# Optimization experiments

Hardware: AMD Instinct MI355X
Metric: run time of the kernel (lower is better)

Reference implementation:

```python
import jax, jax.numpy as jnp
import numpy as np

N = 100000      # nodes
E = 3200000     # edges (avg degree 32)
IN_CH = 32
EDGE_DIM = 11
HID = IN_CH + 4 + EDGE_DIM   # 47
OUT = 128


def setup_inputs() -> dict:
    key = jax.random.key(0)
    ks = jax.random.split(key, 10)
    x = jax.random.normal(ks[0], (N, IN_CH), dtype=jnp.float32)
    pos = jax.random.normal(ks[1], (N, 3), dtype=jnp.float32) * 10.0
    nrm = jax.random.normal(ks[2], (N, 3), dtype=jnp.float32)
    normal = nrm / jnp.linalg.norm(nrm, axis=1, keepdims=True)
    # edges with src != dst (avoids degenerate zero-distance point pairs)
    src = jax.random.randint(ks[3], (E,), 0, N)
    off = jax.random.randint(ks[4], (E,), 1, N)
    dst = (src + off) % N
    edge_index = jnp.stack([src, dst], axis=0).astype(jnp.int64)
    edge_attr = jax.random.normal(ks[5], (E, EDGE_DIM), dtype=jnp.float32)
    W1 = jax.random.normal(ks[6], (HID, HID), dtype=jnp.float32) / np.sqrt(HID)
    b1 = jnp.zeros((HID,), dtype=jnp.float32)
    g1 = jnp.ones((HID,), dtype=jnp.float32)
    be1 = jnp.zeros((HID,), dtype=jnp.float32)
    W2 = jax.random.normal(ks[7], (HID, OUT), dtype=jnp.float32) / np.sqrt(HID)
    b2 = jnp.zeros((OUT,), dtype=jnp.float32)
    g2 = jnp.ones((OUT,), dtype=jnp.float32)
    be2 = jnp.zeros((OUT,), dtype=jnp.float32)
    return {"x": x, "pos": pos, "normal": normal, "edge_attr": edge_attr,
            "W1": W1, "b1": b1, "g1": g1, "be1": be1,
            "W2": W2, "b2": b2, "g2": g2, "be2": be2,
            "edge_index": edge_index}


def _angle(v1, v2):
    return jnp.arctan2(jnp.linalg.norm(jnp.cross(v1, v2), axis=1),
                       jnp.sum(v1 * v2, axis=1))


def _layernorm(h, g, b, eps=1e-5):
    mu = jnp.mean(h, axis=-1, keepdims=True)
    var = jnp.var(h, axis=-1, keepdims=True)  # biased, matches torch LayerNorm
    return (h - mu) / jnp.sqrt(var + eps) * g + b


def reference(x, pos, normal, edge_attr, W1, b1, g1, be1, W2, b2, g2, be2, edge_index):
    src, dst = edge_index[0], edge_index[1]  # message flows src(j) -> dst(i)
    pos_i, pos_j = pos[dst], pos[src]
    n_i, n_j = normal[dst], normal[src]
    x_j = x[src]
    pseudo = pos_j - pos_i                                  # [E,3]
    ppf = jnp.stack([jnp.linalg.norm(pseudo, axis=1),
                     _angle(n_i, pseudo),
                     _angle(n_j, pseudo),
                     _angle(n_i, n_j)], axis=1)             # [E,4]
    msg = jnp.concatenate([x_j, ppf, edge_attr], axis=1)    # [E,47]
    # local_nn = MLP([47,47,128]): (Lin->ReLU->LayerNorm->Dropout(eval)) x2
    h = _layernorm(jax.nn.relu(msg @ W1 + b1), g1, be1)     # [E,47]
    h = _layernorm(jax.nn.relu(h @ W2 + b2), g2, be2)       # [E,128]
    out = jax.ops.segment_max(h, dst, num_segments=N)       # scatter-max per target node
    return jnp.where(jnp.isfinite(out), out, 0.0)           # nodes w/o edges -> 0
```

## Files before the change

kernel.cpp:

```cpp
#include <hip/hip_runtime.h>
#include <cstdint>
#include <cstddef>


typedef _Float16 f16x8 __attribute__((ext_vector_type(8)));
typedef _Float16 f16x2 __attribute__((ext_vector_type(2)));
typedef float    f32x4 __attribute__((ext_vector_type(4)));

#define ENC_NEGINF 0x007FFFFFu
#define LDK 64
#define LDH 132

__device__ __forceinline__ int swz(int row, int col) {
    return (col & 7) | ((((col >> 3) ^ row) & 7) << 3);
}

__device__ __forceinline__ unsigned fenc(float f) {
    unsigned u = __float_as_uint(f);
    return (u & 0x80000000u) ? ~u : (u | 0x80000000u);
}

__global__ void init_out_kernel(unsigned* __restrict__ out, int n4) {
    int i = blockIdx.x * blockDim.x + threadIdx.x;
    if (i < n4)
        ((uint4*)out)[i] = make_uint4(ENC_NEGINF, ENC_NEGINF, ENC_NEGINF, ENC_NEGINF);
}

__global__ void finalize_out_kernel(float* __restrict__ out, int n) {
    int i = blockIdx.x * blockDim.x + threadIdx.x;
    if (i < n) {
        unsigned k = __float_as_uint(out[i]);
        float r;
        if (k == ENC_NEGINF) r = 0.0f;
        else {
            unsigned u = (k & 0x80000000u) ? (k ^ 0x80000000u) : ~k;
            r = __uint_as_float(u);
        }
        out[i] = r;
    }
}

__global__ void zero_kernel(int* __restrict__ p, int n) {
    int i = blockIdx.x * blockDim.x + threadIdx.x;
    if (i < n) p[i] = 0;
}

__global__ void hist_kernel(const int* __restrict__ dstI, int* __restrict__ counts, int E) {
    int i = blockIdx.x * blockDim.x + threadIdx.x;
    if (i < E) atomicAdd(&counts[dstI[i]], 1);
}

__global__ __launch_bounds__(1024) void scan_blk(const int* __restrict__ in,
                                                 int* __restrict__ outp,
                                                 int* __restrict__ bsums, int N) {
    __shared__ int wsum[16];
    const int tid = threadIdx.x, lane = tid & 63, wid = tid >> 6;
    int i = blockIdx.x * 1024 + tid;
    int v = (i < N) ? in[i] : 0;
    int incl = v;
#pragma unroll
    for (int m = 1; m < 64; m <<= 1) {
        int t = __shfl_up(incl, m, 64);
        if (lane >= m) incl += t;
    }
    if (lane == 63) wsum[wid] = incl;
    __syncthreads();
    int woff = 0;
#pragma unroll
    for (int k = 0; k < 16; ++k) woff += (k < wid) ? wsum[k] : 0;
    if (i < N) outp[i] = woff + incl - v;
    if (tid == 1023 && bsums != nullptr) bsums[blockIdx.x] = woff + incl;
}

__global__ __launch_bounds__(1024) void scan_add(int* __restrict__ outp,
                                                 const int* __restrict__ bsums, int N) {
    int i = blockIdx.x * 1024 + threadIdx.x;
    if (i < N) outp[i] += bsums[blockIdx.x];
}

__global__ void scatter_kernel(const int* __restrict__ srcI, const int* __restrict__ dstI,
                               int* __restrict__ nextp,
                               int2* __restrict__ se, int* __restrict__ dst_g, int E) {
    int i = blockIdx.x * blockDim.x + threadIdx.x;
    if (i < E) {
        int d = dstI[i];
        int p = atomicAdd(&nextp[d], 1);
        se[p] = make_int2(srcI[i], i);
        dst_g[p] = d;
    }
}

__global__ __launch_bounds__(512, 4) void edge_kernel_csr(
    const float* __restrict__ x,   const float* __restrict__ pos,
    const float* __restrict__ nrm, const float* __restrict__ ea,
    const float* __restrict__ W1,  const float* __restrict__ b1,
    const float* __restrict__ g1,  const float* __restrict__ be1,
    const float* __restrict__ W2,  const float* __restrict__ b2,
    const float* __restrict__ g2,  const float* __restrict__ be2,
    const int2* __restrict__ se,   const int* __restrict__ dst_g,
    unsigned* __restrict__ out, int E, int ntiles, int tilesPerBlock)
{
    __shared__ _Float16 W1t[48][LDK];
    __shared__ _Float16 W2t[128][LDK];
    __shared__ _Float16 msgA[128][LDK];
    __shared__ _Float16 h2w[128][LDH];
    __shared__ int dstL[128];

    const int lane = threadIdx.x & 63;
    const int w    = threadIdx.x >> 6;
    const int c16  = lane & 15;
    const int g    = lane >> 4;
    const int row0 = w * 16;

    for (int i = threadIdx.x; i < 48 * 64; i += 512) {
        int n = i >> 6, k = i & 63;
        W1t[n][swz(n, k)] = (n < 47 && k < 47) ? (_Float16)W1[k * 47 + n] : (_Float16)0.f;
    }
    for (int i = threadIdx.x; i < 128 * 64; i += 512) {
        int n = i >> 6, k = i & 63;
        W2t[n][swz(n, k)] = (k < 47) ? (_Float16)W2[k * 128 + n] : (_Float16)0.f;
    }
    for (int i = threadIdx.x; i < 128 * LDK; i += 512)
        (&msgA[0][0])[i] = (_Float16)0.f;

    float b1v[3], g1v[3], be1v[3];
#pragma unroll
    for (int n = 0; n < 3; ++n) {
        int cc = n * 16 + c16;
        bool vld = cc < 47;
        b1v[n]  = vld ? b1[cc]  : 0.f;
        g1v[n]  = vld ? g1[cc]  : 0.f;
        be1v[n] = vld ? be1[cc] : 0.f;
    }
    float b2v[8], g2v[8], be2v[8];
#pragma unroll
    for (int n = 0; n < 8; ++n) {
        int cc = n * 16 + c16;
        b2v[n] = b2[cc]; g2v[n] = g2[cc]; be2v[n] = be2[cc];
    }
    __syncthreads();

    const int xr = lane >> 2;
    const int xc = (lane & 3) * 8;
    const int eg = lane / 11, ec = lane - eg * 11;
    const bool ea_act  = lane < 44;
    const bool geo_act = lane < 48;

    const int tbeg = blockIdx.x * tilesPerBlock;
    int tend = tbeg + tilesPerBlock;
    if (tend > ntiles) tend = ntiles;

    for (int tile = tbeg; tile < tend; ++tile) {
        const int base = tile * 128 + row0;

        {
            int p = base + xr;
            bool vx = p < E;
            int s = vx ? se[p].x : 0;
            const float4* xp = (const float4*)(x + (size_t)s * 32 + xc);
            float4 xa = xp[0];
            float4 xb = xp[1];

            float eav0 = 0.f, eav1 = 0.f, eav2 = 0.f, eav3 = 0.f;
            if (ea_act) {
                int p0 = base + 0 * 4 + eg, p1 = base + 1 * 4 + eg;
                int p2 = base + 2 * 4 + eg, p3 = base + 3 * 4 + eg;
                int e0 = (p0 < E) ? se[p0].y : 0;
                int e1 = (p1 < E) ? se[p1].y : 0;
                int e2 = (p2 < E) ? se[p2].y : 0;
                int e3 = (p3 < E) ? se[p3].y : 0;
                eav0 = (p0 < E) ? ea[(size_t)e0 * 11 + ec] : 0.f;
                eav1 = (p1 < E) ? ea[(size_t)e1 * 11 + ec] : 0.f;
                eav2 = (p2 < E) ? ea[(size_t)e2 * 11 + ec] : 0.f;
                eav3 = (p3 < E) ? ea[(size_t)e3 * 11 + ec] : 0.f;
            }

            float gpix = 0.f, gpiy = 0.f, gpiz = 0.f;
            float gpjx = 0.f, gpjy = 0.f, gpjz = 0.f;
            float gnix = 0.f, gniy = 0.f, gniz = 0.f;
            float gnjx = 0.f, gnjy = 0.f, gnjz = 0.f;
            int pd = -1;
            if (geo_act) {
                int pg = base + c16;
                bool v = pg < E;
                int s2 = v ? se[pg].x : 0;
                int d2 = v ? dst_g[pg] : 0;
                pd = v ? d2 : -1;
                gpix = pos[d2 * 3 + 0]; gpiy = pos[d2 * 3 + 1]; gpiz = pos[d2 * 3 + 2];
                gpjx = pos[s2 * 3 + 0]; gpjy = pos[s2 * 3 + 1]; gpjz = pos[s2 * 3 + 2];
                gnix = nrm[d2 * 3 + 0]; gniy = nrm[d2 * 3 + 1]; gniz = nrm[d2 * 3 + 2];
                gnjx = nrm[s2 * 3 + 0]; gnjy = nrm[s2 * 3 + 1]; gnjz = nrm[s2 * 3 + 2];
            }

            {
                int r = row0 + xr;
                f16x8 hv;
                hv[0] = (_Float16)(vx ? xa.x : 0.f); hv[1] = (_Float16)(vx ? xa.y : 0.f);
                hv[2] = (_Float16)(vx ? xa.z : 0.f); hv[3] = (_Float16)(vx ? xa.w : 0.f);
                hv[4] = (_Float16)(vx ? xb.x : 0.f); hv[5] = (_Float16)(vx ? xb.y : 0.f);
                hv[6] = (_Float16)(vx ? xb.z : 0.f); hv[7] = (_Float16)(vx ? xb.w : 0.f);
                *(f16x8*)&msgA[r][swz(r, xc)] = hv;
            }
            if (ea_act) {
                int r0 = row0 + 0 * 4 + eg; msgA[r0][swz(r0, 36 + ec)] = (_Float16)eav0;
                int r1 = row0 + 1 * 4 + eg; msgA[r1][swz(r1, 36 + ec)] = (_Float16)eav1;
                int r2 = row0 + 2 * 4 + eg; msgA[r2][swz(r2, 36 + ec)] = (_Float16)eav2;
                int r3 = row0 + 3 * 4 + eg; msgA[r3][swz(r3, 36 + ec)] = (_Float16)eav3;
            }
            if (geo_act) {
                int r = row0 + c16;
                float px = gpjx - gpix, py = gpjy - gpiy, pz = gpjz - gpiz;
                float v1x, v1y, v1z, v2x, v2y, v2z;
                if (g == 0)      { v1x = gnix; v1y = gniy; v1z = gniz; v2x = px;   v2y = py;   v2z = pz; }
                else if (g == 1) { v1x = gnjx; v1y = gnjy; v1z = gnjz; v2x = px;   v2y = py;   v2z = pz; }
                else             { v1x = gnix; v1y = gniy; v1z = gniz; v2x = gnjx; v2y = gnjy; v2z = gnjz; }
                float cx = v1y * v2z - v1z * v2y;
                float cy = v1z * v2x - v1x * v2z;
                float cz = v1x * v2y - v1y * v2x;
                float ang = atan2f(sqrtf(cx * cx + cy * cy + cz * cz),
                                   v1x * v2x + v1y * v2y + v1z * v2z);
                msgA[r][swz(r, 33 + g)] = (_Float16)ang;
                if (g == 0) {
                    msgA[r][swz(r, 32)] = (_Float16)sqrtf(px * px + py * py + pz * pz);
                    dstL[r] = pd;
                }
            }
        }

        f32x4 acc1[3];
#pragma unroll
        for (int n = 0; n < 3; ++n) acc1[n] = (f32x4){0.f, 0.f, 0.f, 0.f};
#pragma unroll
        for (int ks = 0; ks < 2; ++ks) {
            int ar = row0 + c16;
            f16x8 a = *(const f16x8*)&msgA[ar][swz(ar, ks * 32 + g * 8)];
#pragma unroll
            for (int n = 0; n < 3; ++n) {
                int br = n * 16 + c16;
                f16x8 b = *(const f16x8*)&W1t[br][swz(br, ks * 32 + g * 8)];
                acc1[n] = __builtin_amdgcn_mfma_f32_16x16x32_f16(a, b, acc1[n], 0, 0, 0);
            }
        }
#pragma unroll
        for (int q = 0; q < 4; ++q) {
            float t0 = fmaxf(acc1[0][q] + b1v[0], 0.f);
            float t1 = fmaxf(acc1[1][q] + b1v[1], 0.f);
            float t2 = fmaxf(acc1[2][q] + b1v[2], 0.f);
            float s = t0 + t1 + t2;
            float s2 = t0 * t0 + t1 * t1 + t2 * t2;
#pragma unroll
            for (int m = 1; m < 16; m <<= 1) {
                s  += __shfl_xor(s,  m, 64);
                s2 += __shfl_xor(s2, m, 64);
            }
            float mu  = s * (1.f / 47.f);
            float var = s2 * (1.f / 47.f) - mu * mu;
            float rs  = rsqrtf(var + 1e-5f);
            int r = row0 + 4 * g + q;
            msgA[r][swz(r, c16)]      = (_Float16)((t0 - mu) * rs * g1v[0] + be1v[0]);
            msgA[r][swz(r, 16 + c16)] = (_Float16)((t1 - mu) * rs * g1v[1] + be1v[1]);
            msgA[r][swz(r, 32 + c16)] = (_Float16)((t2 - mu) * rs * g1v[2] + be1v[2]);
        }

        f32x4 acc2[8];
#pragma unroll
        for (int n = 0; n < 8; ++n) acc2[n] = (f32x4){0.f, 0.f, 0.f, 0.f};
#pragma unroll
        for (int ks = 0; ks < 2; ++ks) {
            int ar = row0 + c16;
            f16x8 a = *(const f16x8*)&msgA[ar][swz(ar, ks * 32 + g * 8)];
#pragma unroll
            for (int n = 0; n < 8; ++n) {
                int br = n * 16 + c16;
                f16x8 b = *(const f16x8*)&W2t[br][swz(br, ks * 32 + g * 8)];
                acc2[n] = __builtin_amdgcn_mfma_f32_16x16x32_f16(a, b, acc2[n], 0, 0, 0);
            }
        }
#pragma unroll
        for (int q = 0; q < 4; ++q) {
            float t[8];
            float s = 0.f, s2 = 0.f;
#pragma unroll
            for (int n = 0; n < 8; ++n) {
                t[n] = fmaxf(acc2[n][q] + b2v[n], 0.f);
                s += t[n]; s2 += t[n] * t[n];
            }
#pragma unroll
            for (int m = 1; m < 16; m <<= 1) {
                s  += __shfl_xor(s,  m, 64);
                s2 += __shfl_xor(s2, m, 64);
            }
            float mu  = s * (1.f / 128.f);
            float var = s2 * (1.f / 128.f) - mu * mu;
            float rs  = rsqrtf(var + 1e-5f);
            int r = row0 + 4 * g + q;
#pragma unroll
            for (int n = 0; n < 8; ++n) {
                float o = (t[n] - mu) * rs * g2v[n] + be2v[n];
                h2w[r][n * 16 + c16] = (_Float16)o;
            }
        }

        {
            float m0 = -INFINITY, m1 = -INFINITY;
            int segStart = 0;
            int dcur = dstL[row0];
#pragma unroll
            for (int r = 0; r < 16; ++r) {
                f16x2 pk = *(const f16x2*)&h2w[row0 + r][lane * 2];
                m0 = fmaxf(m0, (float)pk[0]);
                m1 = fmaxf(m1, (float)pk[1]);
                int dnext = (r < 15) ? dstL[row0 + r + 1] : -2;
                if (dnext != dcur) {
                    if (dcur >= 0) {
                        unsigned e0 = fenc(m0), e1 = fenc(m1);
                        unsigned* orow = out + (size_t)dcur * 128 + lane * 2;
                        if (segStart > 0 && r < 15) {
                            unsigned long long pk2 =
                                ((unsigned long long)e1 << 32) | (unsigned long long)e0;
                            *(unsigned long long*)orow = pk2;
                        } else {
                            atomicMax(orow,     e0);
                            atomicMax(orow + 1, e1);
                        }
                    }
                    m0 = -INFINITY; m1 = -INFINITY;
                    segStart = r + 1; dcur = dnext;
                }
            }
        }
    }
}

#define LDKF 72
__global__ __launch_bounds__(256) void edge_kernel_atomic(
    const float* __restrict__ x,   const float* __restrict__ pos,
    const float* __restrict__ nrm, const float* __restrict__ ea,
    const float* __restrict__ W1,  const float* __restrict__ b1,
    const float* __restrict__ g1,  const float* __restrict__ be1,
    const float* __restrict__ W2,  const float* __restrict__ b2,
    const float* __restrict__ g2,  const float* __restrict__ be2,
    const int* __restrict__ srcI,  const int* __restrict__ dstI,
    unsigned* __restrict__ out, int E, int ntiles)
{
    __shared__ _Float16 W1t[48][LDKF];
    __shared__ _Float16 W2t[128][LDKF];
    __shared__ _Float16 msgA[64][LDKF];
    __shared__ int dst_s[64];

    const int lane = threadIdx.x & 63;
    const int w    = threadIdx.x >> 6;
    const int c16  = lane & 15;
    const int g    = lane >> 4;

    for (int i = threadIdx.x; i < 48 * 64; i += 256) {
        int n = i >> 6, k = i & 63;
        W1t[n][k] = (n < 47 && k < 47) ? (_Float16)W1[k * 47 + n] : (_Float16)0.f;
    }
    for (int i = threadIdx.x; i < 128 * 64; i += 256) {
        int n = i >> 6, k = i & 63;
        W2t[n][k] = (k < 47) ? (_Float16)W2[k * 128 + n] : (_Float16)0.f;
    }
    for (int i = threadIdx.x; i < 64 * LDKF; i += 256)
        (&msgA[0][0])[i] = (_Float16)0.f;

    float b1v[3], g1v[3], be1v[3];
#pragma unroll
    for (int n = 0; n < 3; ++n) {
        int cc = n * 16 + c16;
        bool vld = cc < 47;
        b1v[n]  = vld ? b1[cc]  : 0.f;
        g1v[n]  = vld ? g1[cc]  : 0.f;
        be1v[n] = vld ? be1[cc] : 0.f;
    }
    float b2v[8], g2v[8], be2v[8];
#pragma unroll
    for (int n = 0; n < 8; ++n) {
        int cc = n * 16 + c16;
        b2v[n] = b2[cc]; g2v[n] = g2[cc]; be2v[n] = be2[cc];
    }
    __syncthreads();

    for (int tile = blockIdx.x; tile < ntiles; tile += gridDim.x) {
        const int base = tile * 64 + w * 16;
        const int row0 = w * 16;
#pragma unroll
        for (int i = 0; i < 8; ++i) {
            int el = i * 2 + (lane >> 5);
            int e  = base + el;
            int c  = lane & 31;
            float v = 0.f;
            if (e < E) v = x[(size_t)srcI[e] * 32 + c];
            msgA[row0 + el][c] = (_Float16)v;
        }
        if (lane < 44) {
            int eg = lane / 11, c = lane - eg * 11;
#pragma unroll
            for (int i = 0; i < 4; ++i) {
                int el = i * 4 + eg;
                int e  = base + el;
                float v = 0.f;
                if (e < E) v = ea[(size_t)e * 11 + c];
                msgA[row0 + el][36 + c] = (_Float16)v;
            }
        }
        if (lane < 48) {
            int el = c16;
            int e  = base + el;
            int s = 0, d = 0;
            bool vld = e < E;
            if (vld) { s = srcI[e]; d = dstI[e]; }
            float pix = pos[d * 3 + 0], piy = pos[d * 3 + 1], piz = pos[d * 3 + 2];
            float pjx = pos[s * 3 + 0], pjy = pos[s * 3 + 1], pjz = pos[s * 3 + 2];
            float nix = nrm[d * 3 + 0], niy = nrm[d * 3 + 1], niz = nrm[d * 3 + 2];
            float njx = nrm[s * 3 + 0], njy = nrm[s * 3 + 1], njz = nrm[s * 3 + 2];
            float px = pjx - pix, py = pjy - piy, pz = pjz - piz;
            float v1x, v1y, v1z, v2x, v2y, v2z;
            if (g == 0)      { v1x = nix; v1y = niy; v1z = niz; v2x = px;  v2y = py;  v2z = pz;  }
            else if (g == 1) { v1x = njx; v1y = njy; v1z = njz; v2x = px;  v2y = py;  v2z = pz;  }
        else             { v1x = nix; v1y = niy; v1z = niz; v2x = njx; v2y = njy; v2z = njz; }
            float cx = v1y * v2z - v1z * v2y;
            float cy = v1z * v2x - v1x * v2z;
            float cz = v1x * v2y - v1y * v2x;
            float ang = atan2f(sqrtf(cx * cx + cy * cy + cz * cz),
                               v1x * v2x + v1y * v2y + v1z * v2z);
            msgA[row0 + el][33 + g] = (_Float16)ang;
            if (g == 0) {
                msgA[row0 + el][32] = (_Float16)sqrtf(px * px + py * py + pz * pz);
                dst_s[row0 + el] = vld ? d : -1;
            }
        }

        f32x4 acc1[3];
#pragma unroll
        for (int n = 0; n < 3; ++n) acc1[n] = (f32x4){0.f, 0.f, 0.f, 0.f};
#pragma unroll
        for (int ks = 0; ks < 2; ++ks) {
            f16x8 a = *(const f16x8*)&msgA[row0 + c16][ks * 32 + g * 8];
#pragma unroll
            for (int n = 0; n < 3; ++n) {
                f16x8 b = *(const f16x8*)&W1t[n * 16 + c16][ks * 32 + g * 8];
                acc1[n] = __builtin_amdgcn_mfma_f32_16x16x32_f16(a, b, acc1[n], 0, 0, 0);
            }
        }
#pragma unroll
        for (int q = 0; q < 4; ++q) {
            float t0 = fmaxf(acc1[0][q] + b1v[0], 0.f);
            float t1 = fmaxf(acc1[1][q] + b1v[1], 0.f);
            float t2 = fmaxf(acc1[2][q] + b1v[2], 0.f);
            float s = t0 + t1 + t2;
            float s2 = t0 * t0 + t1 * t1 + t2 * t2;
#pragma unroll
            for (int m = 1; m < 16; m <<= 1) {
                s  += __shfl_xor(s,  m, 64);
                s2 += __shfl_xor(s2, m, 64);
            }
            float mu  = s * (1.f / 47.f);
            float var = s2 * (1.f / 47.f) - mu * mu;
            float rs  = rsqrtf(var + 1e-5f);
            int r = row0 + 4 * g + q;
            msgA[r][c16]      = (_Float16)((t0 - mu) * rs * g1v[0] + be1v[0]);
            msgA[r][16 + c16] = (_Float16)((t1 - mu) * rs * g1v[1] + be1v[1]);
            msgA[r][32 + c16] = (_Float16)((t2 - mu) * rs * g1v[2] + be1v[2]);
        }

        f32x4 acc2[8];
#pragma unroll
        for (int n = 0; n < 8; ++n) acc2[n] = (f32x4){0.f, 0.f, 0.f, 0.f};
#pragma unroll
        for (int ks = 0; ks < 2; ++ks) {
            f16x8 a = *(const f16x8*)&msgA[row0 + c16][ks * 32 + g * 8];
#pragma unroll
            for (int n = 0; n < 8; ++n) {
                f16x8 b = *(const f16x8*)&W2t[n * 16 + c16][ks * 32 + g * 8];
                acc2[n] = __builtin_amdgcn_mfma_f32_16x16x32_f16(a, b, acc2[n], 0, 0, 0);
            }
        }
        int4 dd = *(const int4*)&dst_s[row0 + 4 * g];
#pragma unroll
        for (int q = 0; q < 4; ++q) {
            float t[8];
            float s = 0.f, s2 = 0.f;
#pragma unroll
            for (int n = 0; n < 8; ++n) {
                t[n] = fmaxf(acc2[n][q] + b2v[n], 0.f);
                s += t[n]; s2 += t[n] * t[n];
            }
#pragma unroll
            for (int m = 1; m < 16; m <<= 1) {
                s  += __shfl_xor(s,  m, 64);
                s2 += __shfl_xor(s2, m, 64);
            }
            float mu  = s * (1.f / 128.f);
            float var = s2 * (1.f / 128.f) - mu * mu;
            float rs  = rsqrtf(var + 1e-5f);
            int d = (&dd.x)[q];
            if (d >= 0) {
                unsigned* orow = out + (size_t)d * 128u;
#pragma unroll
                for (int n = 0; n < 8; ++n) {
                    float o = (t[n] - mu) * rs * g2v[n] + be2v[n];
                    atomicMax(orow + n * 16 + c16, fenc(o));
                }
            }
        }
    }
}

extern "C" void kernel_launch(void* const* d_in, const int* in_sizes, int n_in,
                              void* d_out, int out_size, void* d_ws, size_t ws_size,
                              hipStream_t stream) {
    const float* x   = (const float*)d_in[0];
    const float* pos = (const float*)d_in[1];
    const float* nrm = (const float*)d_in[2];
    const float* ea  = (const float*)d_in[3];
    const float* W1  = (const float*)d_in[4];
    const float* b1  = (const float*)d_in[5];
    const float* g1  = (const float*)d_in[6];
    const float* be1 = (const float*)d_in[7];
    const float* W2  = (const float*)d_in[8];
    const float* b2  = (const float*)d_in[9];
    const float* g2  = (const float*)d_in[10];
    const float* be2 = (const float*)d_in[11];
    const int*   idx = (const int*)d_in[12];

    const int N = in_sizes[0] / 32;
    const int E = in_sizes[3] / 11;
    const int* srcI = idx;
    const int* dstI = idx + E;

    unsigned* outU = (unsigned*)d_out;
    const int n = N * 128;

    init_out_kernel<<<(n / 4 + 255) / 256, 256, 0, stream>>>(outU, n / 4);

    const int nb = (N + 1023) / 1024;
    const size_t needed = (size_t)E * 8 + (size_t)(2LL * N + E + nb) * 4;

    if (ws_size >= needed) {
        int2* se     = (int2*)d_ws;
        int*  counts = (int*)(se + E);
        int*  nextp  = counts + N;
        int*  dst_g  = nextp + N;
        int*  bsums  = dst_g + E;

        zero_kernel<<<(N + 255) / 256, 256, 0, stream>>>(counts, N);
        hist_kernel<<<(E + 255) / 256, 256, 0, stream>>>(dstI, counts, E);
        scan_blk<<<nb, 1024, 0, stream>>>(counts, nextp, bsums, N);
        scan_blk<<<1, 1024, 0, stream>>>(bsums, bsums, (int*)nullptr, nb);
        scan_add<<<nb, 1024, 0, stream>>>(nextp, bsums, N);
        scatter_kernel<<<(E + 255) / 256, 256, 0, stream>>>(srcI, dstI, nextp,
                                                            se, dst_g, E);

        const int ntiles = (E + 127) / 128;
        int grid = ntiles < 512 ? ntiles : 512;
        int tpb  = (ntiles + grid - 1) / grid;
        edge_kernel_csr<<<grid, 512, 0, stream>>>(x, pos, nrm, ea,
                                                  W1, b1, g1, be1,
                                                  W2, b2, g2, be2,
                                                  se, dst_g,
                                                  outU, E, ntiles, tpb);
    } else {
        const int ntiles = (E + 63) / 64;
        int grid = ntiles < 4096 ? ntiles : 4096;
        edge_kernel_atomic<<<grid, 256, 0, stream>>>(x, pos, nrm, ea,
                                                     W1, b1, g1, be1,
                                                     W2, b2, g2, be2,
                                                     srcI, dstI, outU, E, ntiles);
    }

    finalize_out_kernel<<<(n + 255) / 256, 256, 0, stream>>>((float*)d_out, n);
}
```

Measured before the change: 919.5 us.

## Keep MLP weights in registers, fold biases into GEMM, shrink CSR tiles

```diff
diff --git a/kernel.cpp b/kernel.cpp
--- a/kernel.cpp
+++ b/kernel.cpp
@@ -4,6 +4,7 @@
 
 
 typedef _Float16 f16x8 __attribute__((ext_vector_type(8)));
+typedef _Float16 f16x4 __attribute__((ext_vector_type(4)));
 typedef _Float16 f16x2 __attribute__((ext_vector_type(2)));
 typedef float    f32x4 __attribute__((ext_vector_type(4)));
 
@@ -90,7 +91,7 @@
     }
 }
 
-__global__ __launch_bounds__(512, 4) void edge_kernel_csr(
+__global__ __launch_bounds__(256, 2) void edge_kernel_csr(
     const float* __restrict__ x,   const float* __restrict__ pos,
     const float* __restrict__ nrm, const float* __restrict__ ea,
     const float* __restrict__ W1,  const float* __restrict__ b1,
@@ -98,13 +99,11 @@
     const float* __restrict__ W2,  const float* __restrict__ b2,
     const float* __restrict__ g2,  const float* __restrict__ be2,
     const int2* __restrict__ se,   const int* __restrict__ dst_g,
-    unsigned* __restrict__ out, int E, int ntiles, int tilesPerBlock)
+    unsigned* __restrict__ out, int E, int ntiles)
 {
-    __shared__ _Float16 W1t[48][LDK];
-    __shared__ _Float16 W2t[128][LDK];
-    __shared__ _Float16 msgA[128][LDK];
-    __shared__ _Float16 h2w[128][LDH];
-    __shared__ int dstL[128];
+    __shared__ _Float16 msgA[64][LDK];
+    __shared__ _Float16 h2w[64][LDH];
+    __shared__ int dstL[64];
 
     const int lane = threadIdx.x & 63;
     const int w    = threadIdx.x >> 6;
@@ -112,32 +111,72 @@
     const int g    = lane >> 4;
     const int row0 = w * 16;
 
-    for (int i = threadIdx.x; i < 48 * 64; i += 512) {
-        int n = i >> 6, k = i & 63;
-        W1t[n][swz(n, k)] = (n < 47 && k < 47) ? (_Float16)W1[k * 47 + n] : (_Float16)0.f;
-    }
-    for (int i = threadIdx.x; i < 128 * 64; i += 512) {
-        int n = i >> 6, k = i & 63;
-        W2t[n][swz(n, k)] = (k < 47) ? (_Float16)W2[k * 128 + n] : (_Float16)0.f;
-    }
-    for (int i = threadIdx.x; i < 128 * LDK; i += 512)
+    f16x8 w1a[3][2];
+#pragma unroll
+    for (int j = 0; j < 3; ++j) {
+        int m = j * 16 + c16;
+#pragma unroll
+        for (int ks = 0; ks < 2; ++ks) {
+            f16x8 v;
+#pragma unroll
+            for (int i = 0; i < 8; ++i) {
+                int k = ks * 32 + g * 8 + i;
+                float f = 0.f;
+                if (m < 47) {
+                    if (k < 47)       f = W1[k * 47 + m];
+                    else if (k == 47) f = b1[m];
+                }
+                v[i] = (_Float16)f;
+            }
+            w1a[j][ks] = v;
+        }
+    }
+    f16x8 w2a[8][2];
+#pragma unroll
+    for (int j = 0; j < 8; ++j) {
+        int m = j * 16 + c16;
+#pragma unroll
+        for (int ks = 0; ks < 2; ++ks) {
+            f16x8 v;
+#pragma unroll
+            for (int i = 0; i < 8; ++i) {
+                int k = ks * 32 + g * 8 + i;
+                float f = 0.f;
+                if (k < 47)       f = W2[k * 128 + m];
+                else if (k == 47) f = b2[m];
+                v[i] = (_Float16)f;
+            }
+            w2a[j][ks] = v;
+        }
+    }
+
+    f16x4 g1p[3], be1p[3];
+#pragma unroll
+    for (int j = 0; j < 3; ++j) {
+#pragma unroll
+        for (int q = 0; q < 4; ++q) {
+            int cc = j * 16 + 4 * g + q;
+            bool vld = cc < 47;
+            g1p[j][q]  = (_Float16)(vld ? g1[cc]  : 0.f);
+            be1p[j][q] = (_Float16)(vld ? be1[cc] : 0.f);
+        }
+    }
+    f16x4 g2p[8], be2p[8];
+#pragma unroll
+    for (int j = 0; j < 8; ++j) {
+#pragma unroll
+        for (int q = 0; q < 4; ++q) {
+            int cc = j * 16 + 4 * g + q;
+            g2p[j][q]  = (_Float16)g2[cc];
+            be2p[j][q] = (_Float16)be2[cc];
+        }
+    }
+
+    for (int i = threadIdx.x; i < 64 * LDK; i += 256)
         (&msgA[0][0])[i] = (_Float16)0.f;
-
-    float b1v[3], g1v[3], be1v[3];
-#pragma unroll
-    for (int n = 0; n < 3; ++n) {
-        int cc = n * 16 + c16;
-        bool vld = cc < 47;
-        b1v[n]  = vld ? b1[cc]  : 0.f;
-        g1v[n]  = vld ? g1[cc]  : 0.f;
-        be1v[n] = vld ? be1[cc] : 0.f;
-    }
-    float b2v[8], g2v[8], be2v[8];
-#pragma unroll
-    for (int n = 0; n < 8; ++n) {
-        int cc = n * 16 + c16;
-        b2v[n] = b2[cc]; g2v[n] = g2[cc]; be2v[n] = be2[cc];
-    }
+    __syncthreads();
+    if (threadIdx.x < 64)
+        msgA[threadIdx.x][swz(threadIdx.x, 47)] = (_Float16)1.0f;
     __syncthreads();
 
     const int xr = lane >> 2;
@@ -146,12 +185,8 @@
     const bool ea_act  = lane < 44;
     const bool geo_act = lane < 48;
 
-    const int tbeg = blockIdx.x * tilesPerBlock;
-    int tend = tbeg + tilesPerBlock;
-    if (tend > ntiles) tend = ntiles;
-
-    for (int tile = tbeg; tile < tend; ++tile) {
-        const int base = tile * 128 + row0;
+    for (int tile = blockIdx.x; tile < ntiles; tile += gridDim.x) {
+        const int base = tile * 64 + row0;
 
         {
             int p = base + xr;
@@ -227,77 +262,80 @@
             }
         }
 
+        const int ar = row0 + c16;
+
         f32x4 acc1[3];
 #pragma unroll
-        for (int n = 0; n < 3; ++n) acc1[n] = (f32x4){0.f, 0.f, 0.f, 0.f};
+        for (int j = 0; j < 3; ++j) acc1[j] = (f32x4){0.f, 0.f, 0.f, 0.f};
 #pragma unroll
         for (int ks = 0; ks < 2; ++ks) {
-            int ar = row0 + c16;
-            f16x8 a = *(const f16x8*)&msgA[ar][swz(ar, ks * 32 + g * 8)];
-#pragma unroll
-            for (int n = 0; n < 3; ++n) {
-                int br = n * 16 + c16;
-                f16x8 b = *(const f16x8*)&W1t[br][swz(br, ks * 32 + g * 8)];
-                acc1[n] = __builtin_amdgcn_mfma_f32_16x16x32_f16(a, b, acc1[n], 0, 0, 0);
-            }
-        }
-#pragma unroll
-        for (int q = 0; q < 4; ++q) {
-            float t0 = fmaxf(acc1[0][q] + b1v[0], 0.f);
-            float t1 = fmaxf(acc1[1][q] + b1v[1], 0.f);
-            float t2 = fmaxf(acc1[2][q] + b1v[2], 0.f);
-            float s = t0 + t1 + t2;
-            float s2 = t0 * t0 + t1 * t1 + t2 * t2;
-#pragma unroll
-            for (int m = 1; m < 16; m <<= 1) {
-                s  += __shfl_xor(s,  m, 64);
-                s2 += __shfl_xor(s2, m, 64);
-            }
+            f16x8 bfrag = *(const f16x8*)&msgA[ar][swz(ar, ks * 32 + g * 8)];
+#pragma unroll
+            for (int j = 0; j < 3; ++j)
+                acc1[j] = __builtin_amdgcn_mfma_f32_16x16x32_f16(w1a[j][ks], bfrag, acc1[j], 0, 0, 0);
+        }
+        {
+            float t1v[3][4];
+            float s = 0.f, s2 = 0.f;
+#pragma unroll
+            for (int j = 0; j < 3; ++j)
+#pragma unroll
+                for (int q = 0; q < 4; ++q) {
+                    float t = fmaxf(acc1[j][q], 0.f);
+                    t1v[j][q] = t;
+                    s += t; s2 += t * t;
+                }
+            s  += __shfl_xor(s, 16, 64);  s  += __shfl_xor(s, 32, 64);
+            s2 += __shfl_xor(s2, 16, 64); s2 += __shfl_xor(s2, 32, 64);
             float mu  = s * (1.f / 47.f);
             float var = s2 * (1.f / 47.f) - mu * mu;
             float rs  = rsqrtf(var + 1e-5f);
-            int r = row0 + 4 * g + q;
-            msgA[r][swz(r, c16)]      = (_Float16)((t0 - mu) * rs * g1v[0] + be1v[0]);
-            msgA[r][swz(r, 16 + c16)] = (_Float16)((t1 - mu) * rs * g1v[1] + be1v[1]);
-            msgA[r][swz(r, 32 + c16)] = (_Float16)((t2 - mu) * rs * g1v[2] + be1v[2]);
+#pragma unroll
+            for (int j = 0; j < 3; ++j) {
+                f16x4 hv;
+#pragma unroll
+                for (int q = 0; q < 4; ++q)
+                    hv[q] = (_Float16)((t1v[j][q] - mu) * rs * (float)g1p[j][q]
+                                       + (float)be1p[j][q]);
+                if (j == 2 && g == 3) hv[3] = (_Float16)1.0f;
+                *(f16x4*)&msgA[ar][swz(ar, j * 16 + 4 * g)] = hv;
+            }
         }
 
         f32x4 acc2[8];
 #pragma unroll
-        for (int n = 0; n < 8; ++n) acc2[n] = (f32x4){0.f, 0.f, 0.f, 0.f};
+        for (int j = 0; j < 8; ++j) acc2[j] = (f32x4){0.f, 0.f, 0.f, 0.f};
 #pragma unroll
         for (int ks = 0; ks < 2; ++ks) {
-            int ar = row0 + c16;
-            f16x8 a = *(const f16x8*)&msgA[ar][swz(ar, ks * 32 + g * 8)];
-#pragma unroll
-            for (int n = 0; n < 8; ++n) {
-                int br = n * 16 + c16;
-                f16x8 b = *(const f16x8*)&W2t[br][swz(br, ks * 32 + g * 8)];
-                acc2[n] = __builtin_amdgcn_mfma_f32_16x16x32_f16(a, b, acc2[n], 0, 0, 0);
-            }
-        }
-#pragma unroll
-        for (int q = 0; q < 4; ++q) {
-            float t[8];
+            f16x8 bfrag = *(const f16x8*)&msgA[ar][swz(ar, ks * 32 + g * 8)];
+#pragma unroll
+            for (int j = 0; j < 8; ++j)
+                acc2[j] = __builtin_amdgcn_mfma_f32_16x16x32_f16(w2a[j][ks], bfrag, acc2[j], 0, 0, 0);
+        }
+        {
+            float t2v[8][4];
             float s = 0.f, s2 = 0.f;
 #pragma unroll
-            for (int n = 0; n < 8; ++n) {
-                t[n] = fmaxf(acc2[n][q] + b2v[n], 0.f);
-                s += t[n]; s2 += t[n] * t[n];
-            }
-#pragma unroll
-            for (int m = 1; m < 16; m <<= 1) {
-                s  += __shfl_xor(s,  m, 64);
-                s2 += __shfl_xor(s2, m, 64);
-            }
+            for (int j = 0; j < 8; ++j)
+#pragma unroll
+                for (int q = 0; q < 4; ++q) {
+                    float t = fmaxf(acc2[j][q], 0.f);
+                    t2v[j][q] = t;
+                    s += t; s2 += t * t;
+                }
+            s  += __shfl_xor(s, 16, 64);  s  += __shfl_xor(s, 32, 64);
+            s2 += __shfl_xor(s2, 16, 64); s2 += __shfl_xor(s2, 32, 64);
             float mu  = s * (1.f / 128.f);
             float var = s2 * (1.f / 128.f) - mu * mu;
             float rs  = rsqrtf(var + 1e-5f);
-            int r = row0 + 4 * g + q;
-#pragma unroll
-            for (int n = 0; n < 8; ++n) {
-                float o = (t[n] - mu) * rs * g2v[n] + be2v[n];
-                h2w[r][n * 16 + c16] = (_Float16)o;
+#pragma unroll
+            for (int j = 0; j < 8; ++j) {
+                f16x4 hv;
+#pragma unroll
+                for (int q = 0; q < 4; ++q)
+                    hv[q] = (_Float16)((t2v[j][q] - mu) * rs * (float)g2p[j][q]
+                                       + (float)be2p[j][q]);
+                *(f16x4*)&h2w[ar][j * 16 + 4 * g] = hv;
             }
         }
 
@@ -418,7 +456,7 @@
             float v1x, v1y, v1z, v2x, v2y, v2z;
             if (g == 0)      { v1x = nix; v1y = niy; v1z = niz; v2x = px;  v2y = py;  v2z = pz;  }
             else if (g == 1) { v1x = njx; v1y = njy; v1z = njz; v2x = px;  v2y = py;  v2z = pz;  }
-        else             { v1x = nix; v1y = niy; v1z = niz; v2x = njx; v2y = njy; v2z = njz; }
+            else             { v1x = nix; v1y = niy; v1z = niz; v2x = njx; v2y = njy; v2z = njz; }
             float cx = v1y * v2z - v1z * v2y;
             float cy = v1z * v2x - v1x * v2z;
             float cz = v1x * v2y - v1y * v2x;
@@ -536,6 +574,7 @@
 
     const int nb = (N + 1023) / 1024;
     const size_t needed = (size_t)E * 8 + (size_t)(2LL * N + E + nb) * 4;
+    const int ntiles = (E + 63) / 64;
 
     if (ws_size >= needed) {
         int2* se     = (int2*)d_ws;
@@ -552,16 +591,13 @@
         scatter_kernel<<<(E + 255) / 256, 256, 0, stream>>>(srcI, dstI, nextp,
                                                             se, dst_g, E);
 
-        const int ntiles = (E + 127) / 128;
-        int grid = ntiles < 512 ? ntiles : 512;
-        int tpb  = (ntiles + grid - 1) / grid;
-        edge_kernel_csr<<<grid, 512, 0, stream>>>(x, pos, nrm, ea,
+        int grid = ntiles < 1024 ? ntiles : 1024;
+        edge_kernel_csr<<<grid, 256, 0, stream>>>(x, pos, nrm, ea,
                                                   W1, b1, g1, be1,
                                                   W2, b2, g2, be2,
                                                   se, dst_g,
-                                                  outU, E, ntiles, tpb);
+                                                  outU, E, ntiles);
     } else {
-        const int ntiles = (E + 63) / 64;
         int grid = ntiles < 4096 ? ntiles : 4096;
         edge_kernel_atomic<<<grid, 256, 0, stream>>>(x, pos, nrm, ea,
                                                      W1, b1, g1, be1,
```

Result: slower. 1.521 ms (+65.4%).
